# Kernel tuning notes

Hardware: AMD Instinct MI355X
Metric: run time of the kernel (lower is better)

Reference implementation:

```python
import jax, jax.numpy as jnp
import numpy as np

B, S, NUM_TYPES, NUM_NODES, FREQ = 8, 2048, 8, 32, 256
COMP_R, COMP_L, COMP_C = 0, 1, 2
LS = 0.1  # label smoothing
W_TYPE, W_NODE, W_VAL, W_IMP, W_D1, W_D2, W_SELF, W_DUP = 1.0, 1.0, 0.5, 1.0, 0.5, 0.3, 2.0, 1.0


def setup_inputs() -> dict:
    key = jax.random.key(0)
    ks = jax.random.split(key, 9)
    type_logits = jax.random.normal(ks[0], (B, S, NUM_TYPES), jnp.float32)
    node_a_logits = jax.random.normal(ks[1], (B, S, NUM_NODES), jnp.float32)
    node_b_logits = jax.random.normal(ks[2], (B, S, NUM_NODES), jnp.float32)
    values = jax.random.normal(ks[3], (B, S, 1), jnp.float32)
    t_type = jax.random.randint(ks[4], (B, S, 1), 0, NUM_TYPES)
    t_na = jax.random.randint(ks[5], (B, S, 1), 0, NUM_NODES)
    t_nb = jax.random.randint(ks[6], (B, S, 1), 0, NUM_NODES)
    t_val = jax.random.normal(ks[7], (B, S, 1), jnp.float32)
    target_seq = jnp.concatenate(
        [t_type.astype(jnp.float32), t_na.astype(jnp.float32), t_nb.astype(jnp.float32), t_val], axis=-1)
    ki = jax.random.split(ks[8], 2)
    pred_impedance = jax.random.normal(ki[0], (B, 2, FREQ), jnp.float32)
    target_impedance = jax.random.normal(ki[1], (B, 2, FREQ), jnp.float32)
    return {"type_logits": type_logits, "node_a_logits": node_a_logits,
            "node_b_logits": node_b_logits, "values": values, "target_seq": target_seq,
            "pred_impedance": pred_impedance, "target_impedance": target_impedance}


def _ce_smooth(logits, targets):
    # torch CrossEntropyLoss(label_smoothing=LS), mean reduction
    logp = jax.nn.log_softmax(logits, axis=-1)
    nll = -jnp.take_along_axis(logp, targets[..., None], axis=-1)[..., 0]
    smooth = -jnp.mean(logp, axis=-1)
    return jnp.mean((1.0 - LS) * nll + LS * smooth)


def _mse(a, b):
    return jnp.mean((a - b) ** 2)


def _losses(type_logits, node_a_logits, node_b_logits, values,
            pred_impedance, target_impedance, target_seq):
    target_types = target_seq[:, :, 0].astype(jnp.int32)
    target_na = target_seq[:, :, 1].astype(jnp.int32)
    target_nb = target_seq[:, :, 2].astype(jnp.int32)
    target_values = target_seq[:, :, 3:4]

    type_loss = _ce_smooth(type_logits, target_types)
    node_a_loss = _ce_smooth(node_a_logits, target_na)
    node_b_loss = _ce_smooth(node_b_logits, target_nb)
    value_loss = _mse(values, target_values)

    # validity penalties
    pa = jax.nn.softmax(node_a_logits, axis=-1)  # [B,S,N]
    pb = jax.nn.softmax(node_b_logits, axis=-1)
    pt = jax.nn.softmax(type_logits, axis=-1)
    comp_mask = pt[:, :, COMP_R] + pt[:, :, COMP_L] + pt[:, :, COMP_C]  # [B,S]

    selfloop_prob = jnp.sum(pa * pb, axis=-1)  # [B,S]
    selfloop_penalty = jnp.mean(selfloop_prob * comp_mask)

    # edge_probs[b,s] = outer(pa,pb) + outer(pa,pb).T, flattened to [B,S,N*N]
    outer = jnp.einsum('bsi,bsj->bsij', pa, pb)
    edge = (outer + jnp.swapaxes(outer, -1, -2)).reshape(B, S, NUM_NODES * NUM_NODES)
    em = edge * comp_mask[..., None]  # fold comp weight into edge vectors
    gram = jnp.einsum('bsk,btk->bst', em, em)  # [B,S,S]
    trace = jnp.einsum('bss->b', gram)
    pair_sum = 0.5 * (jnp.sum(gram) - jnp.sum(trace))
    duplicate_penalty = pair_sum / (B * S * (S - 1) / 2 + 1e-8)

    # impedance derivative losses
    pm, tm = pred_impedance[:, 0, :], target_impedance[:, 0, :]
    pp, tp = pred_impedance[:, 1, :], target_impedance[:, 1, :]
    mag_loss = _mse(pm, tm)
    pd1, td1 = pm[:, 1:] - pm[:, :-1], tm[:, 1:] - tm[:, :-1]
    d1_loss = _mse(pd1, td1)
    d2_loss = _mse(pd1[:, 1:] - pd1[:, :-1], td1[:, 1:] - td1[:, :-1])
    phase_loss = _mse(pp, tp)

    total = (W_TYPE * type_loss + W_NODE * (node_a_loss + node_b_loss)
             + W_VAL * value_loss + W_SELF * selfloop_penalty
             + W_DUP * duplicate_penalty + W_IMP * mag_loss
             + W_D1 * d1_loss + W_D2 * d2_loss + 0.1 * phase_loss)
    return (total, type_loss, node_a_loss, node_b_loss, value_loss,
            selfloop_penalty, duplicate_penalty, mag_loss, d1_loss, d2_loss, phase_loss)


def reference(type_logits, node_a_logits, node_b_logits, values, target_seq,
              pred_impedance, target_impedance):
    return _losses(type_logits, node_a_logits, node_b_logits, values,
                   pred_impedance, target_impedance, target_seq)
```

## Files before the change

### kernel.cpp

```cpp
#include <hip/hip_runtime.h>


#define BB 8
#define SS 2048
#define NT 8
#define NN 32
#define FQ 256
#define NPOS (BB*SS)
#define NBLK1 64
#define NSLOT 64
#define NWSLOT 256
#define WS_USLOT 0
#define WS_SSLOT (NSLOT*1024)
#define WS_BATCH (WS_SSLOT + NWSLOT*8)
#define WS_TICKET (WS_BATCH + BB*16)

constexpr float LS_ = 0.1f;

__device__ __forceinline__ float softmax32(const float* __restrict__ src, int pos,
                                           int tgt, float* __restrict__ p) {
    const float4* q = reinterpret_cast<const float4*>(src) + pos * 8;
    #pragma unroll
    for (int i = 0; i < 8; i++) {
        float4 v = q[i];
        p[4*i] = v.x; p[4*i+1] = v.y; p[4*i+2] = v.z; p[4*i+3] = v.w;
    }
    float mx = p[0], sx = 0.f, pt = 0.f;
    #pragma unroll
    for (int i = 0; i < NN; i++) { mx = fmaxf(mx, p[i]); sx += p[i]; }
    #pragma unroll
    for (int i = 0; i < NN; i++) { pt = (i == tgt) ? p[i] : pt; }
    float es = 0.f;
    #pragma unroll
    for (int i = 0; i < NN; i++) { float e = __expf(p[i] - mx); p[i] = e; es += e; }
    const float inv = 1.f / es;
    #pragma unroll
    for (int i = 0; i < NN; i++) p[i] *= inv;
    const float logZ = mx + __logf(es);
    return (1.f - LS_) * (logZ - pt) + LS_ * (logZ - sx * (1.f / NN));
}

__global__ __launch_bounds__(256) void ck_main(
    const float* __restrict__ type_logits,
    const float* __restrict__ na_logits,
    const float* __restrict__ nb_logits,
    const float* __restrict__ values,
    const float* __restrict__ target_seq,
    float* __restrict__ ws)
{
    const int tid  = threadIdx.x;
    const int bid  = blockIdx.x;
    const int w    = tid >> 6;
    const int lane = tid & 63;
    const int b    = bid >> 3;
    const int s    = ((bid & 7) << 8) + tid;
    const int pos  = b * SS + s;
    const int gw   = bid * 4 + w;

    if (tid == 0 && bid == 0) {
        *reinterpret_cast<int*>(ws + WS_TICKET) = 0;
    }

    const float4 tg = reinterpret_cast<const float4*>(target_seq)[pos];
    const float vv = values[pos];
    const int tt = (int)tg.x;
    const int ta = (int)tg.y;
    const int tb = (int)tg.z;
    const float tv = tg.w;

    float x[NT];
    {
        const float4* p = reinterpret_cast<const float4*>(type_logits) + pos * 2;
        float4 v0 = p[0], v1 = p[1];
        x[0]=v0.x; x[1]=v0.y; x[2]=v0.z; x[3]=v0.w;
        x[4]=v1.x; x[5]=v1.y; x[6]=v1.z; x[7]=v1.w;
    }
    float xmax = x[0], xs = 0.f, xt = 0.f;
    #pragma unroll
    for (int i = 0; i < NT; i++) { xmax = fmaxf(xmax, x[i]); xs += x[i]; }
    #pragma unroll
    for (int i = 0; i < NT; i++) { xt = (i == tt) ? x[i] : xt; }
    float es = 0.f, e012 = 0.f;
    #pragma unroll
    for (int i = 0; i < NT; i++) {
        float e = __expf(x[i] - xmax);
        es += e;
        if (i < 3) e012 += e;
    }
    const float logZt = xmax + __logf(es);
    const float lt = (1.f - LS_) * (logZt - xt) + LS_ * (logZt - xs * (1.f / NT));
    const float m = e012 / es;

    float pa[NN], pb[NN];
    const float la = softmax32(na_logits, pos, ta, pa);
    const float lb = softmax32(nb_logits, pos, tb, pb);

    float Sa = 0.f, Sb = 0.f, dot = 0.f;
    #pragma unroll
    for (int i = 0; i < NN; i++) {
        Sa = fmaf(pa[i], pa[i], Sa);
        Sb = fmaf(pb[i], pb[i], Sb);
        dot = fmaf(pa[i], pb[i], dot);
    }
    const float self = m * dot;
    const float tr   = 2.f * m * m * (Sa * Sb + dot * dot);
    const float dv   = vv - tv;
    const float vsq  = dv * dv;

    float r0 = lt, r1 = la, r2 = lb, r3 = vsq, r4 = self, r5 = tr;
    #pragma unroll
    for (int o = 32; o > 0; o >>= 1) {
        r0 += __shfl_down(r0, o); r1 += __shfl_down(r1, o);
        r2 += __shfl_down(r2, o); r3 += __shfl_down(r3, o);
        r4 += __shfl_down(r4, o); r5 += __shfl_down(r5, o);
    }
    if (lane == 0) {
        float* sp = ws + WS_SSLOT + gw * 8;
        sp[0]=r0; sp[1]=r1; sp[2]=r2; sp[3]=r3; sp[4]=r4; sp[5]=r5;
    }

    __shared__ float4 lpa[4][64][9];
    __shared__ float4 lpb[4][64][9];
    #pragma unroll
    for (int q = 0; q < 8; q++) {
        lpa[w][lane][q] = make_float4(m*pa[4*q], m*pa[4*q+1], m*pa[4*q+2], m*pa[4*q+3]);
        lpb[w][lane][q] = make_float4(pb[4*q], pb[4*q+1], pb[4*q+2], pb[4*q+3]);
    }
    __syncthreads();

    const int i4 = lane >> 3;
    const int j4 = lane & 7;
    float acc[4][4];
    #pragma unroll
    for (int ii = 0; ii < 4; ii++)
        #pragma unroll
        for (int jj = 0; jj < 4; jj++) acc[ii][jj] = 0.f;
    for (int t = 0; t < 64; t++) {
        float4 av = lpa[w][t][i4];
        float4 bv = lpb[w][t][j4];
        const float aa[4] = {av.x, av.y, av.z, av.w};
        const float bbv[4] = {bv.x, bv.y, bv.z, bv.w};
        #pragma unroll
        for (int ii = 0; ii < 4; ii++)
            #pragma unroll
            for (int jj = 0; jj < 4; jj++)
                acc[ii][jj] = fmaf(aa[ii], bbv[jj], acc[ii][jj]);
    }

    __shared__ __align__(16) float Ured[4][1024];
    #pragma unroll
    for (int ii = 0; ii < 4; ii++)
        #pragma unroll
        for (int jj = 0; jj < 4; jj++)
            Ured[w][(i4*4+ii)*32 + (j4*4+jj)] = acc[ii][jj];
    __syncthreads();

    {
        const float4* u0 = reinterpret_cast<const float4*>(Ured[0]);
        const float4* u1 = reinterpret_cast<const float4*>(Ured[1]);
        const float4* u2 = reinterpret_cast<const float4*>(Ured[2]);
        const float4* u3 = reinterpret_cast<const float4*>(Ured[3]);
        float4 a = u0[tid], c = u1[tid], d = u2[tid], e = u3[tid];
        float4 sum = make_float4(a.x+c.x+d.x+e.x, a.y+c.y+d.y+e.y,
                                 a.z+c.z+d.z+e.z, a.w+c.w+d.w+e.w);
        reinterpret_cast<float4*>(ws + WS_USLOT + bid * 1024)[tid] = sum;
    }
}

__device__ __forceinline__ float blk_reduce256(float v, float* lds) {
    #pragma unroll
    for (int o = 32; o > 0; o >>= 1) v += __shfl_down(v, o);
    const int tid = threadIdx.x;
    __syncthreads();
    if ((tid & 63) == 0) lds[tid >> 6] = v;
    __syncthreads();
    return lds[0] + lds[1] + lds[2] + lds[3];
}

__global__ __launch_bounds__(256) void ck_batch(
    const float* __restrict__ pred_imp,
    const float* __restrict__ targ_imp,
    float* __restrict__ ws,
    float* __restrict__ out)
{
    const int tid = threadIdx.x;
    const int b   = blockIdx.x;
    __shared__ __align__(16) float Ub[1024];
    __shared__ float red[4];

    const float4* base4 = reinterpret_cast<const float4*>(
        ws + WS_USLOT + (size_t)b * 8 * 1024);
    float4 acc = make_float4(0.f, 0.f, 0.f, 0.f);
    #pragma unroll
    for (int sl = 0; sl < 8; sl++) {
        float4 v = base4[sl * 256 + tid];
        acc.x += v.x; acc.y += v.y; acc.z += v.z; acc.w += v.w;
    }
    reinterpret_cast<float4*>(Ub)[tid] = acc;
    __syncthreads();

    float gr = 0.f;
    #pragma unroll
    for (int r = 0; r < 4; r++) {
        const int e = 4 * tid + r;
        const int i = e >> 5, j = e & 31;
        const float u  = Ub[e];
        const float ut = Ub[(j << 5) | i];
        gr = fmaf(u, u, gr);
        gr = fmaf(u, ut, gr);
    }

    const float* pm = pred_imp + b * 2 * FQ;
    const float* tm = targ_imp + b * 2 * FQ;
    const int f = tid;
    const float p0 = pm[f], t0 = tm[f];
    const float dm = p0 - t0;
    const float dp = pm[FQ + f] - tm[FQ + f];
    float mag = dm * dm;
    float phs = dp * dp;
    float d1 = 0.f, d2 = 0.f;
    if (f < FQ - 1) {
        const float p1 = pm[f + 1], t1 = tm[f + 1];
        const float a = (p1 - p0) - (t1 - t0);
        d1 = a * a;
        if (f < FQ - 2) {
            const float p2 = pm[f + 2], t2 = tm[f + 2];
            const float c = (p2 - 2.f*p1 + p0) - (t2 - 2.f*t1 + t0);
            d2 = c * c;
        }
    }

    float s0=0.f, s1=0.f, s2=0.f, s3=0.f, s4=0.f, s5=0.f;
    if (tid < 32) {
        const float* sp = ws + WS_SSLOT + (b * 32 + tid) * 8;
        s0 = sp[0]; s1 = sp[1]; s2 = sp[2]; s3 = sp[3]; s4 = sp[4]; s5 = sp[5];
    }

    const float GR  = blk_reduce256(gr,  red);
    const float MAG = blk_reduce256(mag, red);
    const float PHS = blk_reduce256(phs, red);
    const float D1  = blk_reduce256(d1,  red);
    const float D2  = blk_reduce256(d2,  red);
    const float S0  = blk_reduce256(s0,  red);
    const float S1  = blk_reduce256(s1,  red);
    const float S2  = blk_reduce256(s2,  red);
    const float S3  = blk_reduce256(s3,  red);
    const float S4  = blk_reduce256(s4,  red);
    const float S5  = blk_reduce256(s5,  red);

    if (tid == 0) {
        float* o = ws + WS_BATCH + b * 16;
        o[0]=GR; o[1]=MAG; o[2]=PHS; o[3]=D1; o[4]=D2;
        o[5]=S0; o[6]=S1; o[7]=S2; o[8]=S3; o[9]=S4; o[10]=S5;

        __threadfence();
        int* ticket = reinterpret_cast<int*>(ws + WS_TICKET);
        const int old = atomicAdd(ticket, 1);
        if (old == BB - 1) {
            __threadfence();
            float GRt=0,MAGt=0,PHSt=0,D1t=0,D2t=0,T0=0,T1=0,T2=0,T3=0,T4=0,T5=0;
            #pragma unroll
            for (int k = 0; k < BB; k++) {
                const float* p = ws + WS_BATCH + k * 16;
                GRt+=p[0]; MAGt+=p[1]; PHSt+=p[2]; D1t+=p[3]; D2t+=p[4];
                T0+=p[5]; T1+=p[6]; T2+=p[7]; T3+=p[8]; T4+=p[9]; T5+=p[10];
            }
            const float invN = 1.f / (float)NPOS;
            const float type_loss = T0 * invN;
            const float na_loss   = T1 * invN;
            const float nb_loss   = T2 * invN;
            const float val_loss  = T3 * invN;
            const float self_p    = T4 * invN;
            const float trace     = T5;
            const float sum_gram  = 2.f * GRt;
            const float pair_sum  = 0.5f * (sum_gram - trace);
            const float dup   = pair_sum / ((float)BB * SS * (SS - 1) * 0.5f + 1e-8f);
            const float mag_l = MAGt / (float)(BB * FQ);
            const float d1_l  = D1t  / (float)(BB * (FQ - 1));
            const float d2_l  = D2t  / (float)(BB * (FQ - 2));
            const float ph_l  = PHSt / (float)(BB * FQ);
            const float total = 1.0f * type_loss + 1.0f * (na_loss + nb_loss)
                              + 0.5f * val_loss + 2.0f * self_p + 1.0f * dup
                              + 1.0f * mag_l + 0.5f * d1_l + 0.3f * d2_l + 0.1f * ph_l;
            out[0]=total; out[1]=type_loss; out[2]=na_loss; out[3]=nb_loss;
            out[4]=val_loss; out[5]=self_p; out[6]=dup; out[7]=mag_l;
            out[8]=d1_l; out[9]=d2_l; out[10]=ph_l;
        }
    }
}

extern "C" void kernel_launch(void* const* d_in, const int* in_sizes, int n_in,
                              void* d_out, int out_size, void* d_ws, size_t ws_size,
                              hipStream_t stream)
{
    const float* type_logits = (const float*)d_in[0];
    const float* na_logits   = (const float*)d_in[1];
    const float* nb_logits   = (const float*)d_in[2];
    const float* values      = (const float*)d_in[3];
    const float* target_seq  = (const float*)d_in[4];
    const float* pred_imp    = (const float*)d_in[5];
    const float* targ_imp    = (const float*)d_in[6];
    float* out = (float*)d_out;
    float* ws  = (float*)d_ws;

    ck_main<<<NBLK1, 256, 0, stream>>>(type_logits, na_logits, nb_logits,
                                       values, target_seq, ws);
    ck_batch<<<BB, 256, 0, stream>>>(pred_imp, targ_imp, ws, out);
}
```

Measured before the change: 79.85 us.

## Fuse main and batch-reduction kernels into one launch with last-block finalization

Merges the two kernels into a single kernel. Each block reduces its per-warp scalar partials in shared memory before writing one slot, blocks 0-7 also compute the impedance losses, and an atomic ticket picks the last block to run the Gram reduction and write the final outputs. This removes the second kernel launch and its dependency gap. In exchange, one block now does all eight batches' Gram reduction serially, reading the whole partial buffer alone. The ticket is never reset in the kernel; it only works if the workspace is re-poisoned with 0xAA (or zeroed) before every call.

```diff
diff --git a/kernel.cpp b/kernel.cpp
--- a/kernel.cpp
+++ b/kernel.cpp
@@ -7,13 +7,12 @@
 #define NN 32
 #define FQ 256
 #define NPOS (BB*SS)
-#define NBLK1 64
-#define NSLOT 64
-#define NWSLOT 256
+#define NBLK 64
 #define WS_USLOT 0
-#define WS_SSLOT (NSLOT*1024)
-#define WS_BATCH (WS_SSLOT + NWSLOT*8)
-#define WS_TICKET (WS_BATCH + BB*16)
+#define WS_SSLOT (NBLK*1024)
+#define WS_IMP   (WS_SSLOT + NBLK*8)
+#define WS_TICKET (WS_IMP + BB*4)
+#define POISON_INT ((int)0xAAAAAAAA)
 
 constexpr float LS_ = 0.1f;
 
@@ -40,13 +39,26 @@
     return (1.f - LS_) * (logZ - pt) + LS_ * (logZ - sx * (1.f / NN));
 }
 
-__global__ __launch_bounds__(256) void ck_main(
+__device__ __forceinline__ float blk_reduce256(float v, float* lds) {
+    #pragma unroll
+    for (int o = 32; o > 0; o >>= 1) v += __shfl_down(v, o);
+    const int tid = threadIdx.x;
+    __syncthreads();
+    if ((tid & 63) == 0) lds[tid >> 6] = v;
+    __syncthreads();
+    return lds[0] + lds[1] + lds[2] + lds[3];
+}
+
+__global__ __launch_bounds__(256) void ck_fused(
     const float* __restrict__ type_logits,
     const float* __restrict__ na_logits,
     const float* __restrict__ nb_logits,
     const float* __restrict__ values,
     const float* __restrict__ target_seq,
-    float* __restrict__ ws)
+    const float* __restrict__ pred_imp,
+    const float* __restrict__ targ_imp,
+    float* __restrict__ ws,
+    float* __restrict__ out)
 {
     const int tid  = threadIdx.x;
     const int bid  = blockIdx.x;
@@ -55,11 +67,15 @@
     const int b    = bid >> 3;
     const int s    = ((bid & 7) << 8) + tid;
     const int pos  = b * SS + s;
-    const int gw   = bid * 4 + w;
-
-    if (tid == 0 && bid == 0) {
-        *reinterpret_cast<int*>(ws + WS_TICKET) = 0;
-    }
+
+    __shared__ __align__(16) char smem[90112];
+    float4* lpa  = reinterpret_cast<float4*>(smem);
+    float4* lpb  = reinterpret_cast<float4*>(smem + 36864);
+    float*  ured = reinterpret_cast<float*>(smem + 73728);
+    float*  uall = reinterpret_cast<float*>(smem);
+    __shared__ float sred[4][8];
+    __shared__ float red[4];
+    __shared__ int lastflag;
 
     const float4 tg = reinterpret_cast<const float4*>(target_seq)[pos];
     const float vv = values[pos];
@@ -115,18 +131,23 @@
         r4 += __shfl_down(r4, o); r5 += __shfl_down(r5, o);
     }
     if (lane == 0) {
-        float* sp = ws + WS_SSLOT + gw * 8;
-        sp[0]=r0; sp[1]=r1; sp[2]=r2; sp[3]=r3; sp[4]=r4; sp[5]=r5;
-    }
-
-    __shared__ float4 lpa[4][64][9];
-    __shared__ float4 lpb[4][64][9];
+        sred[w][0]=r0; sred[w][1]=r1; sred[w][2]=r2;
+        sred[w][3]=r3; sred[w][4]=r4; sred[w][5]=r5;
+    }
+
+    float4* wpa = lpa + w * 576 + lane * 9;
+    float4* wpb = lpb + w * 576 + lane * 9;
     #pragma unroll
     for (int q = 0; q < 8; q++) {
-        lpa[w][lane][q] = make_float4(m*pa[4*q], m*pa[4*q+1], m*pa[4*q+2], m*pa[4*q+3]);
-        lpb[w][lane][q] = make_float4(pb[4*q], pb[4*q+1], pb[4*q+2], pb[4*q+3]);
-    }
-    __syncthreads();
+        wpa[q] = make_float4(m*pa[4*q], m*pa[4*q+1], m*pa[4*q+2], m*pa[4*q+3]);
+        wpb[q] = make_float4(pb[4*q], pb[4*q+1], pb[4*q+2], pb[4*q+3]);
+    }
+    __syncthreads();
+
+    if (tid < 6) {
+        float* sp = ws + WS_SSLOT + bid * 8;
+        sp[tid] = sred[0][tid] + sred[1][tid] + sred[2][tid] + sred[3][tid];
+    }
 
     const int i4 = lane >> 3;
     const int j4 = lane & 7;
@@ -136,8 +157,8 @@
         #pragma unroll
         for (int jj = 0; jj < 4; jj++) acc[ii][jj] = 0.f;
     for (int t = 0; t < 64; t++) {
-        float4 av = lpa[w][t][i4];
-        float4 bv = lpb[w][t][j4];
+        float4 av = lpa[w * 576 + t * 9 + i4];
+        float4 bv = lpb[w * 576 + t * 9 + j4];
         const float aa[4] = {av.x, av.y, av.z, av.w};
         const float bbv[4] = {bv.x, bv.y, bv.z, bv.w};
         #pragma unroll
@@ -147,145 +168,135 @@
                 acc[ii][jj] = fmaf(aa[ii], bbv[jj], acc[ii][jj]);
     }
 
-    __shared__ __align__(16) float Ured[4][1024];
     #pragma unroll
     for (int ii = 0; ii < 4; ii++)
         #pragma unroll
         for (int jj = 0; jj < 4; jj++)
-            Ured[w][(i4*4+ii)*32 + (j4*4+jj)] = acc[ii][jj];
-    __syncthreads();
-
+            ured[w * 1024 + (i4*4+ii)*32 + (j4*4+jj)] = acc[ii][jj];
+    __syncthreads();
     {
-        const float4* u0 = reinterpret_cast<const float4*>(Ured[0]);
-        const float4* u1 = reinterpret_cast<const float4*>(Ured[1]);
-        const float4* u2 = reinterpret_cast<const float4*>(Ured[2]);
-        const float4* u3 = reinterpret_cast<const float4*>(Ured[3]);
-        float4 a = u0[tid], c = u1[tid], d = u2[tid], e = u3[tid];
+        const float4* u0 = reinterpret_cast<const float4*>(ured);
+        float4 a = u0[tid], c = u0[256+tid], d = u0[512+tid], e = u0[768+tid];
         float4 sum = make_float4(a.x+c.x+d.x+e.x, a.y+c.y+d.y+e.y,
                                  a.z+c.z+d.z+e.z, a.w+c.w+d.w+e.w);
         reinterpret_cast<float4*>(ws + WS_USLOT + bid * 1024)[tid] = sum;
     }
-}
-
-__device__ __forceinline__ float blk_reduce256(float v, float* lds) {
-    #pragma unroll
-    for (int o = 32; o > 0; o >>= 1) v += __shfl_down(v, o);
-    const int tid = threadIdx.x;
-    __syncthreads();
-    if ((tid & 63) == 0) lds[tid >> 6] = v;
-    __syncthreads();
-    return lds[0] + lds[1] + lds[2] + lds[3];
-}
-
-__global__ __launch_bounds__(256) void ck_batch(
-    const float* __restrict__ pred_imp,
-    const float* __restrict__ targ_imp,
-    float* __restrict__ ws,
-    float* __restrict__ out)
-{
-    const int tid = threadIdx.x;
-    const int b   = blockIdx.x;
-    __shared__ __align__(16) float Ub[1024];
-    __shared__ float red[4];
-
-    const float4* base4 = reinterpret_cast<const float4*>(
-        ws + WS_USLOT + (size_t)b * 8 * 1024);
-    float4 acc = make_float4(0.f, 0.f, 0.f, 0.f);
-    #pragma unroll
-    for (int sl = 0; sl < 8; sl++) {
-        float4 v = base4[sl * 256 + tid];
-        acc.x += v.x; acc.y += v.y; acc.z += v.z; acc.w += v.w;
-    }
-    reinterpret_cast<float4*>(Ub)[tid] = acc;
+
+    if (bid < BB) {
+        const float* pm = pred_imp + bid * 2 * FQ;
+        const float* tm = targ_imp + bid * 2 * FQ;
+        const int f = tid;
+        const float p0 = pm[f], t0 = tm[f];
+        const float dm = p0 - t0;
+        const float dp = pm[FQ + f] - tm[FQ + f];
+        float mag = dm * dm;
+        float phs = dp * dp;
+        float d1 = 0.f, d2 = 0.f;
+        if (f < FQ - 1) {
+            const float p1 = pm[f + 1], t1 = tm[f + 1];
+            const float a = (p1 - p0) - (t1 - t0);
+            d1 = a * a;
+            if (f < FQ - 2) {
+                const float p2 = pm[f + 2], t2 = tm[f + 2];
+                const float c = (p2 - 2.f*p1 + p0) - (t2 - 2.f*t1 + t0);
+                d2 = c * c;
+            }
+        }
+        const float MAG = blk_reduce256(mag, red);
+        const float PHS = blk_reduce256(phs, red);
+        const float D1  = blk_reduce256(d1,  red);
+        const float D2  = blk_reduce256(d2,  red);
+        if (tid == 0) {
+            float* ip = ws + WS_IMP + bid * 4;
+            ip[0]=MAG; ip[1]=PHS; ip[2]=D1; ip[3]=D2;
+        }
+    }
+
+    __threadfence();
+    if (tid == 0) {
+        int* ticket = reinterpret_cast<int*>(ws + WS_TICKET);
+        const int old = atomicAdd(ticket, 1);
+        lastflag = (old == POISON_INT + (NBLK - 1)) || (old == NBLK - 1);
+    }
+    __syncthreads();
+    if (!lastflag) return;
+
+    __threadfence();
+
+    {
+        const float4* g = reinterpret_cast<const float4*>(ws + WS_USLOT);
+        #pragma unroll
+        for (int bb = 0; bb < BB; bb++) {
+            float4 acc4 = make_float4(0.f, 0.f, 0.f, 0.f);
+            #pragma unroll
+            for (int sl = 0; sl < 8; sl++) {
+                float4 v = g[(bb * 8 + sl) * 256 + tid];
+                acc4.x += v.x; acc4.y += v.y; acc4.z += v.z; acc4.w += v.w;
+            }
+            reinterpret_cast<float4*>(uall + bb * 1024)[tid] = acc4;
+        }
+    }
     __syncthreads();
 
     float gr = 0.f;
     #pragma unroll
-    for (int r = 0; r < 4; r++) {
-        const int e = 4 * tid + r;
-        const int i = e >> 5, j = e & 31;
-        const float u  = Ub[e];
-        const float ut = Ub[(j << 5) | i];
-        gr = fmaf(u, u, gr);
-        gr = fmaf(u, ut, gr);
-    }
-
-    const float* pm = pred_imp + b * 2 * FQ;
-    const float* tm = targ_imp + b * 2 * FQ;
-    const int f = tid;
-    const float p0 = pm[f], t0 = tm[f];
-    const float dm = p0 - t0;
-    const float dp = pm[FQ + f] - tm[FQ + f];
-    float mag = dm * dm;
-    float phs = dp * dp;
-    float d1 = 0.f, d2 = 0.f;
-    if (f < FQ - 1) {
-        const float p1 = pm[f + 1], t1 = tm[f + 1];
-        const float a = (p1 - p0) - (t1 - t0);
-        d1 = a * a;
-        if (f < FQ - 2) {
-            const float p2 = pm[f + 2], t2 = tm[f + 2];
-            const float c = (p2 - 2.f*p1 + p0) - (t2 - 2.f*t1 + t0);
-            d2 = c * c;
+    for (int bb = 0; bb < BB; bb++) {
+        const float* ub = uall + bb * 1024;
+        #pragma unroll
+        for (int r = 0; r < 4; r++) {
+            const int e = 4 * tid + r;
+            const int i = e >> 5, j = e & 31;
+            const float u  = ub[e];
+            const float ut = ub[(j << 5) | i];
+            gr = fmaf(u, u, gr);
+            gr = fmaf(u, ut, gr);
         }
     }
 
     float s0=0.f, s1=0.f, s2=0.f, s3=0.f, s4=0.f, s5=0.f;
-    if (tid < 32) {
-        const float* sp = ws + WS_SSLOT + (b * 32 + tid) * 8;
-        s0 = sp[0]; s1 = sp[1]; s2 = sp[2]; s3 = sp[3]; s4 = sp[4]; s5 = sp[5];
+    if (tid < NBLK) {
+        const float* sp = ws + WS_SSLOT + tid * 8;
+        s0=sp[0]; s1=sp[1]; s2=sp[2]; s3=sp[3]; s4=sp[4]; s5=sp[5];
+    }
+    float mg=0.f, ph=0.f, dd1=0.f, dd2=0.f;
+    if (tid < BB) {
+        const float* ip = ws + WS_IMP + tid * 4;
+        mg=ip[0]; ph=ip[1]; dd1=ip[2]; dd2=ip[3];
     }
 
     const float GR  = blk_reduce256(gr,  red);
-    const float MAG = blk_reduce256(mag, red);
-    const float PHS = blk_reduce256(phs, red);
-    const float D1  = blk_reduce256(d1,  red);
-    const float D2  = blk_reduce256(d2,  red);
     const float S0  = blk_reduce256(s0,  red);
     const float S1  = blk_reduce256(s1,  red);
     const float S2  = blk_reduce256(s2,  red);
     const float S3  = blk_reduce256(s3,  red);
     const float S4  = blk_reduce256(s4,  red);
     const float S5  = blk_reduce256(s5,  red);
+    const float MAG = blk_reduce256(mg,  red);
+    const float PHS = blk_reduce256(ph,  red);
+    const float D1  = blk_reduce256(dd1, red);
+    const float D2  = blk_reduce256(dd2, red);
 
     if (tid == 0) {
-        float* o = ws + WS_BATCH + b * 16;
-        o[0]=GR; o[1]=MAG; o[2]=PHS; o[3]=D1; o[4]=D2;
-        o[5]=S0; o[6]=S1; o[7]=S2; o[8]=S3; o[9]=S4; o[10]=S5;
-
-        __threadfence();
-        int* ticket = reinterpret_cast<int*>(ws + WS_TICKET);
-        const int old = atomicAdd(ticket, 1);
-        if (old == BB - 1) {
-            __threadfence();
-            float GRt=0,MAGt=0,PHSt=0,D1t=0,D2t=0,T0=0,T1=0,T2=0,T3=0,T4=0,T5=0;
-            #pragma unroll
-            for (int k = 0; k < BB; k++) {
-                const float* p = ws + WS_BATCH + k * 16;
-                GRt+=p[0]; MAGt+=p[1]; PHSt+=p[2]; D1t+=p[3]; D2t+=p[4];
-                T0+=p[5]; T1+=p[6]; T2+=p[7]; T3+=p[8]; T4+=p[9]; T5+=p[10];
-            }
-            const float invN = 1.f / (float)NPOS;
-            const float type_loss = T0 * invN;
-            const float na_loss   = T1 * invN;
-            const float nb_loss   = T2 * invN;
-            const float val_loss  = T3 * invN;
-            const float self_p    = T4 * invN;
-            const float trace     = T5;
-            const float sum_gram  = 2.f * GRt;
-            const float pair_sum  = 0.5f * (sum_gram - trace);
-            const float dup   = pair_sum / ((float)BB * SS * (SS - 1) * 0.5f + 1e-8f);
-            const float mag_l = MAGt / (float)(BB * FQ);
-            const float d1_l  = D1t  / (float)(BB * (FQ - 1));
-            const float d2_l  = D2t  / (float)(BB * (FQ - 2));
-            const float ph_l  = PHSt / (float)(BB * FQ);
-            const float total = 1.0f * type_loss + 1.0f * (na_loss + nb_loss)
-                              + 0.5f * val_loss + 2.0f * self_p + 1.0f * dup
-                              + 1.0f * mag_l + 0.5f * d1_l + 0.3f * d2_l + 0.1f * ph_l;
-            out[0]=total; out[1]=type_loss; out[2]=na_loss; out[3]=nb_loss;
-            out[4]=val_loss; out[5]=self_p; out[6]=dup; out[7]=mag_l;
-            out[8]=d1_l; out[9]=d2_l; out[10]=ph_l;
-        }
+        const float invN = 1.f / (float)NPOS;
+        const float type_loss = S0 * invN;
+        const float na_loss   = S1 * invN;
+        const float nb_loss   = S2 * invN;
+        const float val_loss  = S3 * invN;
+        const float self_p    = S4 * invN;
+        const float trace     = S5;
+        const float sum_gram  = 2.f * GR;
+        const float pair_sum  = 0.5f * (sum_gram - trace);
+        const float dup   = pair_sum / ((float)BB * SS * (SS - 1) * 0.5f + 1e-8f);
+        const float mag_l = MAG / (float)(BB * FQ);
+        const float d1_l  = D1  / (float)(BB * (FQ - 1));
+        const float d2_l  = D2  / (float)(BB * (FQ - 2));
+        const float ph_l  = PHS / (float)(BB * FQ);
+        const float total = 1.0f * type_loss + 1.0f * (na_loss + nb_loss)
+                          + 0.5f * val_loss + 2.0f * self_p + 1.0f * dup
+                          + 1.0f * mag_l + 0.5f * d1_l + 0.3f * d2_l + 0.1f * ph_l;
+        out[0]=total; out[1]=type_loss; out[2]=na_loss; out[3]=nb_loss;
+        out[4]=val_loss; out[5]=self_p; out[6]=dup; out[7]=mag_l;
+        out[8]=d1_l; out[9]=d2_l; out[10]=ph_l;
     }
 }
 
@@ -303,7 +314,7 @@
     float* out = (float*)d_out;
     float* ws  = (float*)d_ws;
 
-    ck_main<<<NBLK1, 256, 0, stream>>>(type_logits, na_logits, nb_logits,
-                                       values, target_seq, ws);
-    ck_batch<<<BB, 256, 0, stream>>>(pred_imp, targ_imp, ws, out);
+    ck_fused<<<NBLK, 256, 0, stream>>>(type_logits, na_logits, nb_logits,
+                                       values, target_seq, pred_imp, targ_imp,
+                                       ws, out);
 }
```

Measured after the change: 86.34 us. +8.1%, slower.
